# Kernel tuning notes

Measured on AMD Instinct MI355X. Metric: run time of the kernel, lower is better.

## Reference

```python
import jax, jax.numpy as jnp
import numpy as np
import math

EPS = 1e-5

def _ln(x, g, b):
    m = jnp.mean(x, axis=-1, keepdims=True)
    v = jnp.var(x, axis=-1, keepdims=True)
    return (x - m) * jax.lax.rsqrt(v + EPS) * g + b

def _rn_layer(x, W, g, b, A, Bb, Rw):
    # x: (B,S,in) -> (B,S,out). W: (out,in), A: (out,basis), Bb: (basis,out)
    S = x.shape[1]
    basis_dim = Bb.shape[0]
    n = _ln(x @ W.T, g, b)                      # (B,S,out)
    j = jnp.arange(S) % basis_dim               # (S,)
    Bv = Bb[j]                                  # (S,out)
    scal = jnp.einsum('bsd,sd->bs', n, Bv)      # (B,S)
    Av = A[:, j].T                              # (S,out)
    nf = scal[..., None] * Av                   # (B,S,out)
    res = x if Rw is None else x @ Rw.T
    return nf + res

def _ts_layer(x, M, g, b, P, Rw):
    # x: (B,S,in) -> (B,S,out). M: (out,in), P: (out,out,G)
    S = x.shape[1]
    D, _, G = P.shape
    t = _ln(x @ M.T, g, b)                      # (B,S,out)
    k = jnp.arange(S, dtype=jnp.float32)
    periods = (jnp.arange(D, dtype=jnp.float32)[:, None, None] * (D * G)
               + jnp.arange(D, dtype=jnp.float32)[None, :, None] * G
               + jnp.arange(G, dtype=jnp.float32)[None, None, :] + 2.0)  # (D,D,G)
    phi = jnp.cos(2.0 * math.pi * k[:, None, None, None] / periods)       # (S,D,D,G)
    # Nk[b,s,i] = sum_{j,g} P[i,j,g] * t[b,s,j] * phi[s,i,j,g]
    Wp = jnp.einsum('ijg,sijg->sij', P, phi)    # (S,D,D)
    Nk = jnp.einsum('sij,bsj->bsi', Wp, t)      # (B,S,D)
    return Nk + x @ Rw.T

def setup_inputs() -> dict:
    key = jax.random.key(0)
    ks = jax.random.split(key, 16)
    B, S = 2, 2048
    d0, d1, d2 = 512, 64, 512        # input_dim, ts out, final out
    bas1, G, bas3 = 64, 8, 64
    u = lambda k, sh, a: jax.random.uniform(k, sh, jnp.float32, -a, a)
    inp = {
        'x':  jax.random.normal(ks[0], (B, S, d0), jnp.float32),
        # Layer 1: RN 512->512 (in==out -> no residual proj)
        'W1': u(ks[1], (d0, d0), 0.1),
        'g1': jnp.ones((d0,), jnp.float32),
        'b1': jnp.zeros((d0,), jnp.float32),
        'A1': u(ks[2], (d0, bas1), 0.1),
        'B1': u(ks[3], (bas1, d0), 0.1),
        # Layer 2: TS 512->64
        'M2': u(ks[4], (d1, d0), 0.5),
        'g2': jnp.ones((d1,), jnp.float32),
        'b2': jnp.zeros((d1,), jnp.float32),
        'P2': u(ks[5], (d1, d1, G), 0.1),
        'R2': u(ks[6], (d1, d0), 0.1),
        # Layer 3: RN 64->512
        'W3': u(ks[7], (d2, d1), 0.1),
        'g3': jnp.ones((d2,), jnp.float32),
        'b3': jnp.zeros((d2,), jnp.float32),
        'A3': u(ks[8], (d2, bas3), 0.1),
        'B3': u(ks[9], (bas3, d2), 0.1),
        'R3': u(ks[10], (d2, d1), 0.1),
    }
    return inp

def reference(x, W1, g1, b1, A1, B1, M2, g2, b2, P2, R2, W3, g3, b3, A3, B3, R3):
    h = _rn_layer(x, W1, g1, b1, A1, B1, None)   # (B,S,512), identity residual
    h = _ts_layer(h, M2, g2, b2, P2, R2)         # (B,S,64)
    h = _rn_layer(h, W3, g3, b3, A3, B3, R3)     # (B,S,512)
    return h
```

## Files before the change

kernel.cpp:

```cpp
#include <hip/hip_runtime.h>
#include <math.h>

#define SEQ  2048
#define ROWS 4096
#define D0   512
#define D1   64

typedef short bf8 __attribute__((ext_vector_type(8)));
typedef float f4  __attribute__((ext_vector_type(4)));

__device__ __forceinline__ unsigned short f2bf(float f) {
    unsigned u = __float_as_uint(f);
    return (unsigned short)((u + 0x7fffu + ((u >> 16) & 1u)) >> 16);
}
__device__ __forceinline__ void hilo(float f, unsigned short& h, unsigned short& l) {
    h = f2bf(f);
    float fh = __uint_as_float((unsigned)h << 16);
    l = f2bf(f - fh);
}
__device__ __forceinline__ void cv4(unsigned short* dh, unsigned short* dl, int idx, float4 v) {
    ushort4 hv, lv;
    hilo(v.x, hv.x, lv.x); hilo(v.y, hv.y, lv.y);
    hilo(v.z, hv.z, lv.z); hilo(v.w, hv.w, lv.w);
    *(ushort4*)(dh + idx) = hv;
    *(ushort4*)(dl + idx) = lv;
}

__device__ __forceinline__ void async16(const void* g, void* l) {
    __builtin_amdgcn_global_load_lds(
        (const __attribute__((address_space(1))) unsigned int*)g,
        (__attribute__((address_space(3))) unsigned int*)l, 16, 0, 0);
}

__global__ __launch_bounds__(256) void convk(
        const float* __restrict__ x,  const float* __restrict__ W1,
        const float* __restrict__ M2, const float* __restrict__ R2,
        const float* __restrict__ W3, const float* __restrict__ R3,
        const float* __restrict__ A1, const float* __restrict__ A3,
        unsigned short* __restrict__ xh,  unsigned short* __restrict__ xl,
        unsigned short* __restrict__ W1h, unsigned short* __restrict__ W1l,
        unsigned short* __restrict__ C2h, unsigned short* __restrict__ C2l,
        unsigned short* __restrict__ C3h, unsigned short* __restrict__ C3l,
        float* __restrict__ A1T, float* __restrict__ A3T) {
    int c = blockIdx.x, tid = threadIdx.x;
    if (c < 1216) {
        const float* src; unsigned short *dh, *dl; int off;
        if      (c < 1024) { src = x;  dh = xh;          dl = xl;          off = c; }
        else if (c < 1152) { src = W1; dh = W1h;         dl = W1l;         off = c - 1024; }
        else if (c < 1168) { src = M2; dh = C2h;         dl = C2l;         off = c - 1152; }
        else if (c < 1184) { src = R2; dh = C2h + 32768; dl = C2l + 32768; off = c - 1168; }
        else if (c < 1200) { src = W3; dh = C3h;         dl = C3l;         off = c - 1184; }
        else               { src = R3; dh = C3h + 32768; dl = C3l + 32768; off = c - 1200; }
        int base = off * 2048 + tid * 4;
        cv4(dh, dl, base,        *(const float4*)(src + base));
        cv4(dh, dl, base + 1024, *(const float4*)(src + base + 1024));
    } else {
        int gid = (c - 1216) * 256 + tid;
        int i = gid >> 6, j = gid & 63;
        A1T[j * 512 + i] = A1[gid];
        A3T[j * 512 + i] = A3[gid];
    }
}

__global__ __launch_bounds__(256, 4) void gemm64(
        const unsigned short* __restrict__ Ah, const unsigned short* __restrict__ Al,
        const unsigned short* __restrict__ Wh, const unsigned short* __restrict__ Wl,
        float* __restrict__ C, int M, int N, int K, int Ks) {
    __shared__ __align__(16) unsigned short aH[4096], aL[4096], wH[4096], wL[4096];
    const int tid = threadIdx.x;
    const int wv  = tid >> 6;
    const int ln  = tid & 63;
    const int lm  = ln & 15;
    const int lq  = ln >> 4;
    const int bm  = blockIdx.y * 64;
    const int bn  = blockIdx.x * 64;
    const int k0  = blockIdx.z * Ks;
    C += (size_t)blockIdx.z * M * N;

    f4 acc[4] = {};

    for (int kt = 0; kt < Ks; kt += 64) {
        const int kg = k0 + kt;
        __syncthreads();
#pragma unroll
        for (int i = 0; i < 2; ++i) {
            int slot = i * 256 + wv * 64 + ln;
            int row  = slot >> 3;
            int ch   = (slot & 7) ^ (row & 7);
            size_t goA = (size_t)(bm + row) * K + kg + ch * 8;
            size_t goW = (size_t)(bn + row) * K + kg + ch * 8;
            async16(Ah + goA, aH + slot * 8);
            async16(Al + goA, aL + slot * 8);
            async16(Wh + goW, wH + slot * 8);
            async16(Wl + goW, wL + slot * 8);
        }
        __syncthreads();

#pragma unroll
        for (int kk = 0; kk < 2; ++kk) {
            const int ck = kk * 4 + lq;
            const int r  = wv * 16 + lm;
            bf8 ah = *(const bf8*)(aH + r * 64 + ((ck ^ (r & 7)) * 8));
            bf8 al = *(const bf8*)(aL + r * 64 + ((ck ^ (r & 7)) * 8));
            bf8 bh[4], bl[4];
#pragma unroll
            for (int u = 0; u < 4; ++u) {
                int rb = u * 16 + lm;
                bh[u] = *(const bf8*)(wH + rb * 64 + ((ck ^ (rb & 7)) * 8));
                bl[u] = *(const bf8*)(wL + rb * 64 + ((ck ^ (rb & 7)) * 8));
            }
#pragma unroll
            for (int u = 0; u < 4; ++u) {
                acc[u] = __builtin_amdgcn_mfma_f32_16x16x32_bf16(ah, bh[u], acc[u], 0, 0, 0);
                acc[u] = __builtin_amdgcn_mfma_f32_16x16x32_bf16(ah, bl[u], acc[u], 0, 0, 0);
                acc[u] = __builtin_amdgcn_mfma_f32_16x16x32_bf16(al, bh[u], acc[u], 0, 0, 0);
            }
        }
    }

#pragma unroll
    for (int u = 0; u < 4; ++u) {
        int row = bm + wv * 16 + lq * 4;
        int col = bn + u * 16 + lm;
#pragma unroll
        for (int r = 0; r < 4; ++r)
            C[(size_t)(row + r) * N + col] = acc[u][r];
    }
}

__global__ __launch_bounds__(256) void lnrn(
        const float* __restrict__ Y, const float* __restrict__ Y2, int ldy,
        const float* __restrict__ RES, int ldr,
        const float* __restrict__ g, const float* __restrict__ be,
        const float* __restrict__ Bb, const float* __restrict__ AaT,
        float* __restrict__ outf,
        unsigned short* __restrict__ outh, unsigned short* __restrict__ outl) {
    const int row = blockIdx.x * 4 + (threadIdx.x >> 6);
    const int l = threadIdx.x & 63;
    const int c = l * 8;
    const float* y = Y + (size_t)row * ldy + c;
    float4 y0 = *(const float4*)y;
    float4 y1 = *(const float4*)(y + 4);
    if (Y2) {
        const float* y2 = Y2 + (size_t)row * ldy + c;
        float4 p0 = *(const float4*)y2, p1 = *(const float4*)(y2 + 4);
        y0.x += p0.x; y0.y += p0.y; y0.z += p0.z; y0.w += p0.w;
        y1.x += p1.x; y1.y += p1.y; y1.z += p1.z; y1.w += p1.w;
    }
    float sum = y0.x + y0.y + y0.z + y0.w + y1.x + y1.y + y1.z + y1.w;
    float ssq = y0.x*y0.x + y0.y*y0.y + y0.z*y0.z + y0.w*y0.w
              + y1.x*y1.x + y1.y*y1.y + y1.z*y1.z + y1.w*y1.w;
#pragma unroll
    for (int m = 1; m < 64; m <<= 1) {
        sum += __shfl_xor(sum, m, 64);
        ssq += __shfl_xor(ssq, m, 64);
    }
    float mean = sum * (1.0f / 512.0f);
    float var  = ssq * (1.0f / 512.0f) - mean * mean;
    float rstd = rsqrtf(var + 1e-5f);
    float4 g0 = *(const float4*)(g + c),  g1v = *(const float4*)(g + c + 4);
    float4 e0 = *(const float4*)(be + c), e1  = *(const float4*)(be + c + 4);
    float4 n0, n1;
    n0.x = (y0.x - mean) * rstd * g0.x  + e0.x;
    n0.y = (y0.y - mean) * rstd * g0.y  + e0.y;
    n0.z = (y0.z - mean) * rstd * g0.z  + e0.z;
    n0.w = (y0.w - mean) * rstd * g0.w  + e0.w;
    n1.x = (y1.x - mean) * rstd * g1v.x + e1.x;
    n1.y = (y1.y - mean) * rstd * g1v.y + e1.y;
    n1.z = (y1.z - mean) * rstd * g1v.z + e1.z;
    n1.w = (y1.w - mean) * rstd * g1v.w + e1.w;
    const int jm = row & 63;
    const float* bb = Bb + jm * D0 + c;
    float4 b0 = *(const float4*)bb, b1v = *(const float4*)(bb + 4);
    float p = n0.x*b0.x + n0.y*b0.y + n0.z*b0.z + n0.w*b0.w
            + n1.x*b1v.x + n1.y*b1v.y + n1.z*b1v.z + n1.w*b1v.w;
#pragma unroll
    for (int m = 1; m < 64; m <<= 1) p += __shfl_xor(p, m, 64);
    const float* av = AaT + jm * D0 + c;
    float4 a0 = *(const float4*)av, a1 = *(const float4*)(av + 4);
    const float* rs = RES + (size_t)row * ldr + c;
    float4 r0 = *(const float4*)rs, r1 = *(const float4*)(rs + 4);
    float4 v0, v1;
    v0.x = p*a0.x + r0.x; v0.y = p*a0.y + r0.y; v0.z = p*a0.z + r0.z; v0.w = p*a0.w + r0.w;
    v1.x = p*a1.x + r1.x; v1.y = p*a1.y + r1.y; v1.z = p*a1.z + r1.z; v1.w = p*a1.w + r1.w;
    if (outf) {
        *(float4*)(outf + (size_t)row * D0 + c)     = v0;
        *(float4*)(outf + (size_t)row * D0 + c + 4) = v1;
    } else {
        ushort4 h0, l0, h1, l1;
        hilo(v0.x, h0.x, l0.x); hilo(v0.y, h0.y, l0.y);
        hilo(v0.z, h0.z, l0.z); hilo(v0.w, h0.w, l0.w);
        hilo(v1.x, h1.x, l1.x); hilo(v1.y, h1.y, l1.y);
        hilo(v1.z, h1.z, l1.z); hilo(v1.w, h1.w, l1.w);
        *(ushort4*)(outh + (size_t)row * D0 + c)     = h0;
        *(ushort4*)(outl + (size_t)row * D0 + c)     = l0;
        *(ushort4*)(outh + (size_t)row * D0 + c + 4) = h1;
        *(ushort4*)(outl + (size_t)row * D0 + c + 4) = l1;
    }
}

#define C2S 524288
__global__ __launch_bounds__(256) void lnt(
        const float* __restrict__ C2, const float* __restrict__ g2,
        const float* __restrict__ b2,
        float* __restrict__ t, float* __restrict__ rsum) {
    const int r = blockIdx.x * 4 + (threadIdx.x >> 6);
    const int j = threadIdx.x & 63;
    size_t base = (size_t)r * 128 + j;
    float v = 0.f, rv = 0.f;
#pragma unroll
    for (int z = 0; z < 4; ++z) {
        v  += C2[(size_t)z * C2S + base];
        rv += C2[(size_t)z * C2S + base + 64];
    }
    float sum = v, ssq = v * v;
#pragma unroll
    for (int m = 1; m < 64; m <<= 1) {
        sum += __shfl_xor(sum, m, 64);
        ssq += __shfl_xor(ssq, m, 64);
    }
    float mean = sum * (1.0f / 64.0f);
    float var  = ssq * (1.0f / 64.0f) - mean * mean;
    float rstd = rsqrtf(var + 1e-5f);
    t[r * 64 + j]    = (v - mean) * rstd * g2[j] + b2[j];
    rsum[r * 64 + j] = rv;
}

__global__ __launch_bounds__(256) void tsk2(
        const float* __restrict__ t, const float* __restrict__ rsum,
        const float* __restrict__ P,
        unsigned short* __restrict__ Hh, unsigned short* __restrict__ Hl) {
    const int bid = blockIdx.x;
    const int i   = bid >> 3;
    const int sg  = bid & 7;
    const int w   = threadIdx.x >> 6;
    const int ln  = threadIdx.x & 63;
    const int s0  = sg * 256 + w * 64;
    const int idx = i * 64 + ln;
    const float* pp = P + idx * 8;
    const float sf0 = (float)s0;

    float k2c[8], ca[8], cb[8];
#pragma unroll
    for (int g = 0; g < 8; ++g) {
        float pf   = (float)(idx * 8 + g + 2);
        float invp = __builtin_amdgcn_rcpf(pf);
        k2c[g] = 2.0f * __builtin_amdgcn_cosf(invp);
        float q0 = floorf(sf0 * invp);
        float r0 = fmaf(-q0, pf, sf0);
        float f0 = r0 * invp; f0 -= floorf(f0);
        float c0 = __builtin_amdgcn_cosf(f0);
        float sf1 = sf0 + 1.0f;
        float q1 = floorf(sf1 * invp);
        float r1 = fmaf(-q1, pf, sf1);
        float f1 = r1 * invp; f1 -= floorf(f1);
        float c1 = __builtin_amdgcn_cosf(f1);
        float Pv = pp[g];
        ca[g] = Pv * c0;
        cb[g] = Pv * c1;
    }

    const int tb = s0 * 64 + ln;
    float t0c = t[tb], t1c = t[131072 + tb];
    float res0 = 0.f, res1 = 0.f;

    for (int st = 0; st < 64; st += 2) {
        float t0n  = t[tb + (st + 1) * 64];
        float t1n  = t[131072 + tb + (st + 1) * 64];
        float ws = ((ca[0] + ca[1]) + (ca[2] + ca[3]))
                 + ((ca[4] + ca[5]) + (ca[6] + ca[7]));
#pragma unroll
        for (int g = 0; g < 8; ++g) ca[g] = fmaf(k2c[g], cb[g], -ca[g]);
        float v0 = ws * t0c, v1 = ws * t1c;
#pragma unroll
        for (int m = 1; m < 64; m <<= 1) {
            v0 += __shfl_xor(v0, m, 64);
            v1 += __shfl_xor(v1, m, 64);
        }
        res0 = (ln == st) ? v0 : res0;
        res1 = (ln == st) ? v1 : res1;
        float t0n2 = t[tb + (st + 2) * 64];
        float t1n2 = t[131072 + tb + (st + 2) * 64];
        float ws2 = ((cb[0] + cb[1]) + (cb[2] + cb[3]))
                  + ((cb[4] + cb[5]) + (cb[6] + cb[7]));
#pragma unroll
        for (int g = 0; g < 8; ++g) cb[g] = fmaf(k2c[g], ca[g], -cb[g]);
        float v0b = ws2 * t0n, v1b = ws2 * t1n;
#pragma unroll
        for (int m = 1; m < 64; m <<= 1) {
            v0b += __shfl_xor(v0b, m, 64);
            v1b += __shfl_xor(v1b, m, 64);
        }
        res0 = (ln == st + 1) ? v0b : res0;
        res1 = (ln == st + 1) ? v1b : res1;
        t0c = t0n2; t1c = t1n2;
    }

    const int s = s0 + ln;
    {
        float v = res0 + rsum[(size_t)s * 64 + i];
        unsigned short h, l; hilo(v, h, l);
        Hh[(size_t)s * 64 + i] = h; Hl[(size_t)s * 64 + i] = l;
        float v1e = res1 + rsum[(size_t)(SEQ + s) * 64 + i];
        hilo(v1e, h, l);
        Hh[(size_t)(SEQ + s) * 64 + i] = h; Hl[(size_t)(SEQ + s) * 64 + i] = l;
    }
}

extern "C" void kernel_launch(void* const* d_in, const int* in_sizes, int n_in,
                              void* d_out, int out_size, void* d_ws, size_t ws_size,
                              hipStream_t stream) {
    const float* x  = (const float*)d_in[0];
    const float* W1 = (const float*)d_in[1];
    const float* g1 = (const float*)d_in[2];
    const float* b1 = (const float*)d_in[3];
    const float* A1 = (const float*)d_in[4];
    const float* B1 = (const float*)d_in[5];
    const float* M2 = (const float*)d_in[6];
    const float* g2 = (const float*)d_in[7];
    const float* b2 = (const float*)d_in[8];
    const float* P2 = (const float*)d_in[9];
    const float* R2 = (const float*)d_in[10];
    const float* W3 = (const float*)d_in[11];
    const float* g3 = (const float*)d_in[12];
    const float* b3 = (const float*)d_in[13];
    const float* A3 = (const float*)d_in[14];
    const float* B3 = (const float*)d_in[15];
    const float* R3 = (const float*)d_in[16];

    float* ws = (float*)d_ws;
    float* C1   = ws;
    float* C2   = ws + 4194304;
    float* C3   = ws + 6291456;
    float* t    = ws + 10485760;
    float* rsum = ws + 10747904;
    float* A1T  = ws + 11010048;
    float* A3T  = ws + 11042816;
    unsigned short* us = (unsigned short*)(ws + 11075584);
    unsigned short* xh   = us;
    unsigned short* xl   = us + 2097152;
    unsigned short* h1h  = us + 4194304;
    unsigned short* h1l  = us + 6291456;
    unsigned short* W1h  = us + 8388608;
    unsigned short* W1l  = us + 8650752;
    unsigned short* Wc2h = us + 8912896;
    unsigned short* Wc2l = us + 8978432;
    unsigned short* Wc3h = us + 9043968;
    unsigned short* Wc3l = us + 9109504;
    unsigned short* h2h  = us + 9175040;
    unsigned short* h2l  = us + 9437184;

    dim3 blk(256);

    convk<<<1344, blk, 0, stream>>>(x, W1, M2, R2, W3, R3, A1, A3,
                                    xh, xl, W1h, W1l, Wc2h, Wc2l, Wc3h, Wc3l,
                                    A1T, A3T);

    gemm64<<<dim3(8, 64, 2), blk, 0, stream>>>(xh, xl, W1h, W1l, C1, ROWS, 512, 512, 256);
    lnrn<<<1024, blk, 0, stream>>>(C1, C1 + 2097152, 512, x, 512, g1, b1, B1, A1T,
                                   nullptr, h1h, h1l);

    gemm64<<<dim3(2, 64, 4), blk, 0, stream>>>(h1h, h1l, Wc2h, Wc2l, C2, ROWS, 128, 512, 128);
    lnt<<<1024, blk, 0, stream>>>(C2, g2, b2, t, rsum);
    tsk2<<<512, blk, 0, stream>>>(t, rsum, P2, h2h, h2l);

    gemm64<<<dim3(16, 64, 1), blk, 0, stream>>>(h2h, h2l, Wc3h, Wc3l, C3, ROWS, 1024, 64, 64);
    lnrn<<<1024, blk, 0, stream>>>(C3, nullptr, 1024, C3 + 512, 1024, g3, b3, B3, A3T,
                                   (float*)d_out, nullptr, nullptr);
}
```

Before: 159.1 us.

## Drop weight low-bf16 split and enlarge GEMM M-tile to 128 rows

Weights are now converted only to a high bf16 part, so the split-precision GEMM does two MFMAs per tile (ah*bh, al*bh) instead of three and no longer loads the weight low halves. The GEMM block tile grows from 64 to 128 rows, so each wave computes a 32x64 output and reuses each weight fragment across two A fragments. This cuts MFMA count, global traffic and conversion work. In exchange, weight precision drops to plain bf16, and the larger tile halves the number of blocks and raises LDS and register use.

```diff
diff --git a/kernel.cpp b/kernel.cpp
--- a/kernel.cpp
+++ b/kernel.cpp
@@ -25,6 +25,11 @@
     *(ushort4*)(dh + idx) = hv;
     *(ushort4*)(dl + idx) = lv;
 }
+__device__ __forceinline__ void cv4h(unsigned short* dh, int idx, float4 v) {
+    ushort4 hv;
+    hv.x = f2bf(v.x); hv.y = f2bf(v.y); hv.z = f2bf(v.z); hv.w = f2bf(v.w);
+    *(ushort4*)(dh + idx) = hv;
+}
 
 __device__ __forceinline__ void async16(const void* g, void* l) {
     __builtin_amdgcn_global_load_lds(
@@ -38,22 +43,25 @@
         const float* __restrict__ W3, const float* __restrict__ R3,
         const float* __restrict__ A1, const float* __restrict__ A3,
         unsigned short* __restrict__ xh,  unsigned short* __restrict__ xl,
-        unsigned short* __restrict__ W1h, unsigned short* __restrict__ W1l,
-        unsigned short* __restrict__ C2h, unsigned short* __restrict__ C2l,
-        unsigned short* __restrict__ C3h, unsigned short* __restrict__ C3l,
+        unsigned short* __restrict__ W1h,
+        unsigned short* __restrict__ C2h,
+        unsigned short* __restrict__ C3h,
         float* __restrict__ A1T, float* __restrict__ A3T) {
     int c = blockIdx.x, tid = threadIdx.x;
-    if (c < 1216) {
-        const float* src; unsigned short *dh, *dl; int off;
-        if      (c < 1024) { src = x;  dh = xh;          dl = xl;          off = c; }
-        else if (c < 1152) { src = W1; dh = W1h;         dl = W1l;         off = c - 1024; }
-        else if (c < 1168) { src = M2; dh = C2h;         dl = C2l;         off = c - 1152; }
-        else if (c < 1184) { src = R2; dh = C2h + 32768; dl = C2l + 32768; off = c - 1168; }
-        else if (c < 1200) { src = W3; dh = C3h;         dl = C3l;         off = c - 1184; }
-        else               { src = R3; dh = C3h + 32768; dl = C3l + 32768; off = c - 1200; }
+    if (c < 1024) {
+        int base = c * 2048 + tid * 4;
+        cv4(xh, xl, base,        *(const float4*)(x + base));
+        cv4(xh, xl, base + 1024, *(const float4*)(x + base + 1024));
+    } else if (c < 1216) {
+        const float* src; unsigned short* dh; int off;
+        if      (c < 1152) { src = W1; dh = W1h;         off = c - 1024; }
+        else if (c < 1168) { src = M2; dh = C2h;         off = c - 1152; }
+        else if (c < 1184) { src = R2; dh = C2h + 32768; off = c - 1168; }
+        else if (c < 1200) { src = W3; dh = C3h;         off = c - 1184; }
+        else               { src = R3; dh = C3h + 32768; off = c - 1200; }
         int base = off * 2048 + tid * 4;
-        cv4(dh, dl, base,        *(const float4*)(src + base));
-        cv4(dh, dl, base + 1024, *(const float4*)(src + base + 1024));
+        cv4h(dh, base,        *(const float4*)(src + base));
+        cv4h(dh, base + 1024, *(const float4*)(src + base + 1024));
     } else {
         int gid = (c - 1216) * 256 + tid;
         int i = gid >> 6, j = gid & 63;
@@ -62,70 +70,80 @@
     }
 }
 
-__global__ __launch_bounds__(256, 4) void gemm64(
+__global__ __launch_bounds__(256, 4) void gemm128(
         const unsigned short* __restrict__ Ah, const unsigned short* __restrict__ Al,
-        const unsigned short* __restrict__ Wh, const unsigned short* __restrict__ Wl,
+        const unsigned short* __restrict__ Wh,
         float* __restrict__ C, int M, int N, int K, int Ks) {
-    __shared__ __align__(16) unsigned short aH[4096], aL[4096], wH[4096], wL[4096];
+    __shared__ __align__(16) unsigned short aH[8192], aL[8192], wH[4096];
     const int tid = threadIdx.x;
     const int wv  = tid >> 6;
     const int ln  = tid & 63;
     const int lm  = ln & 15;
     const int lq  = ln >> 4;
-    const int bm  = blockIdx.y * 64;
+    const int bm  = blockIdx.y * 128;
     const int bn  = blockIdx.x * 64;
     const int k0  = blockIdx.z * Ks;
     C += (size_t)blockIdx.z * M * N;
 
-    f4 acc[4] = {};
+    f4 acc[2][4] = {};
 
     for (int kt = 0; kt < Ks; kt += 64) {
         const int kg = k0 + kt;
         __syncthreads();
+#pragma unroll
+        for (int i = 0; i < 4; ++i) {
+            int slot = i * 256 + wv * 64 + ln;
+            int row  = slot >> 3;
+            int ch   = (slot & 7) ^ (row & 7);
+            size_t go = (size_t)(bm + row) * K + kg + ch * 8;
+            async16(Ah + go, aH + slot * 8);
+            async16(Al + go, aL + slot * 8);
+        }
 #pragma unroll
         for (int i = 0; i < 2; ++i) {
             int slot = i * 256 + wv * 64 + ln;
             int row  = slot >> 3;
             int ch   = (slot & 7) ^ (row & 7);
-            size_t goA = (size_t)(bm + row) * K + kg + ch * 8;
-            size_t goW = (size_t)(bn + row) * K + kg + ch * 8;
-            async16(Ah + goA, aH + slot * 8);
-            async16(Al + goA, aL + slot * 8);
-            async16(Wh + goW, wH + slot * 8);
-            async16(Wl + goW, wL + slot * 8);
+            size_t go = (size_t)(bn + row) * K + kg + ch * 8;
+            async16(Wh + go, wH + slot * 8);
         }
         __syncthreads();
 
 #pragma unroll
         for (int kk = 0; kk < 2; ++kk) {
             const int ck = kk * 4 + lq;
-            const int r  = wv * 16 + lm;
-            bf8 ah = *(const bf8*)(aH + r * 64 + ((ck ^ (r & 7)) * 8));
-            bf8 al = *(const bf8*)(aL + r * 64 + ((ck ^ (r & 7)) * 8));
-            bf8 bh[4], bl[4];
+            bf8 a_h[2], a_l[2], b_h[4];
+#pragma unroll
+            for (int t = 0; t < 2; ++t) {
+                int r = wv * 32 + t * 16 + lm;
+                a_h[t] = *(const bf8*)(aH + r * 64 + ((ck ^ (r & 7)) * 8));
+                a_l[t] = *(const bf8*)(aL + r * 64 + ((ck ^ (r & 7)) * 8));
+            }
 #pragma unroll
             for (int u = 0; u < 4; ++u) {
                 int rb = u * 16 + lm;
-                bh[u] = *(const bf8*)(wH + rb * 64 + ((ck ^ (rb & 7)) * 8));
-                bl[u] = *(const bf8*)(wL + rb * 64 + ((ck ^ (rb & 7)) * 8));
+                b_h[u] = *(const bf8*)(wH + rb * 64 + ((ck ^ (rb & 7)) * 8));
             }
 #pragma unroll
-            for (int u = 0; u < 4; ++u) {
-                acc[u] = __builtin_amdgcn_mfma_f32_16x16x32_bf16(ah, bh[u], acc[u], 0, 0, 0);
-                acc[u] = __builtin_amdgcn_mfma_f32_16x16x32_bf16(ah, bl[u], acc[u], 0, 0, 0);
-                acc[u] = __builtin_amdgcn_mfma_f32_16x16x32_bf16(al, bh[u], acc[u], 0, 0, 0);
-            }
-        }
-    }
-
-#pragma unroll
-    for (int u = 0; u < 4; ++u) {
-        int row = bm + wv * 16 + lq * 4;
-        int col = bn + u * 16 + lm;
-#pragma unroll
-        for (int r = 0; r < 4; ++r)
-            C[(size_t)(row + r) * N + col] = acc[u][r];
-    }
+            for (int t = 0; t < 2; ++t)
+#pragma unroll
+                for (int u = 0; u < 4; ++u) {
+                    acc[t][u] = __builtin_amdgcn_mfma_f32_16x16x32_bf16(a_h[t], b_h[u], acc[t][u], 0, 0, 0);
+                    acc[t][u] = __builtin_amdgcn_mfma_f32_16x16x32_bf16(a_l[t], b_h[u], acc[t][u], 0, 0, 0);
+                }
+        }
+    }
+
+#pragma unroll
+    for (int t = 0; t < 2; ++t)
+#pragma unroll
+        for (int u = 0; u < 4; ++u) {
+            int row = bm + wv * 32 + t * 16 + lq * 4;
+            int col = bn + u * 16 + lm;
+#pragma unroll
+            for (int r = 0; r < 4; ++r)
+                C[(size_t)(row + r) * N + col] = acc[t][u][r];
+        }
 }
 
 __global__ __launch_bounds__(256) void lnrn(
@@ -342,29 +360,25 @@
     unsigned short* h1h  = us + 4194304;
     unsigned short* h1l  = us + 6291456;
     unsigned short* W1h  = us + 8388608;
-    unsigned short* W1l  = us + 8650752;
-    unsigned short* Wc2h = us + 8912896;
-    unsigned short* Wc2l = us + 8978432;
-    unsigned short* Wc3h = us + 9043968;
-    unsigned short* Wc3l = us + 9109504;
-    unsigned short* h2h  = us + 9175040;
-    unsigned short* h2l  = us + 9437184;
+    unsigned short* Wc2h = us + 8650752;
+    unsigned short* Wc3h = us + 8716288;
+    unsigned short* h2h  = us + 8781824;
+    unsigned short* h2l  = us + 9043968;
 
     dim3 blk(256);
 
     convk<<<1344, blk, 0, stream>>>(x, W1, M2, R2, W3, R3, A1, A3,
-                                    xh, xl, W1h, W1l, Wc2h, Wc2l, Wc3h, Wc3l,
-                                    A1T, A3T);
-
-    gemm64<<<dim3(8, 64, 2), blk, 0, stream>>>(xh, xl, W1h, W1l, C1, ROWS, 512, 512, 256);
+                                    xh, xl, W1h, Wc2h, Wc3h, A1T, A3T);
+
+    gemm128<<<dim3(8, 32, 2), blk, 0, stream>>>(xh, xl, W1h, C1, ROWS, 512, 512, 256);
     lnrn<<<1024, blk, 0, stream>>>(C1, C1 + 2097152, 512, x, 512, g1, b1, B1, A1T,
                                    nullptr, h1h, h1l);
 
-    gemm64<<<dim3(2, 64, 4), blk, 0, stream>>>(h1h, h1l, Wc2h, Wc2l, C2, ROWS, 128, 512, 128);
+    gemm128<<<dim3(2, 32, 4), blk, 0, stream>>>(h1h, h1l, Wc2h, C2, ROWS, 128, 512, 128);
     lnt<<<1024, blk, 0, stream>>>(C2, g2, b2, t, rsum);
     tsk2<<<512, blk, 0, stream>>>(t, rsum, P2, h2h, h2l);
 
-    gemm64<<<dim3(16, 64, 1), blk, 0, stream>>>(h2h, h2l, Wc3h, Wc3l, C3, ROWS, 1024, 64, 64);
+    gemm128<<<dim3(16, 32, 1), blk, 0, stream>>>(h2h, h2l, Wc3h, C3, ROWS, 1024, 64, 64);
     lnrn<<<1024, blk, 0, stream>>>(C3, nullptr, 1024, C3 + 512, 1024, g3, b3, B3, A3T,
                                    (float*)d_out, nullptr, nullptr);
 }
```

Result: no change. 160.7 us (+1.0%).
